# Performance work log

Hardware: AMD Instinct MI355X
Metric: run time of the kernel (lower is better)

## Reference

```python
import jax, jax.numpy as jnp
import numpy as np

H, W = 480, 640
N, Q, K = 128, 8192, 10
MIN_DEPTH = 0.1


def setup_inputs() -> dict:
    key = jax.random.key(0)
    ks = jax.random.split(key, 8)
    pred_depth = jax.random.uniform(ks[0], (1, H, W), jnp.float32, 0.5, 10.0)
    gt_depth = jax.random.uniform(ks[1], (1, H, W), jnp.float32, 0.0, 10.0)
    gt_masks = jax.random.uniform(ks[2], (N, H, W)) > 0.5
    random_mask = jax.random.uniform(ks[3], (N, H, W)) > 0.95  # matches torch.rand>0.95
    k_matrix = jnp.array([[500.0, 0.0, W / 2.0], [0.0, 500.0, H / 2.0], [0.0, 0.0, 1.0]], jnp.float32)
    xq = jax.random.randint(ks[4], (N, Q), 0, H, jnp.int32)
    yq = jax.random.randint(ks[5], (N, Q), 0, W, jnp.int32)
    xp = jax.random.randint(ks[6], (N, K), 0, H, jnp.int32)
    yp = jax.random.randint(ks[7], (N, K), 0, W, jnp.int32)
    return {"pred_depth": pred_depth, "gt_masks": gt_masks, "gt_depth": gt_depth,
            "k_matrix": k_matrix, "random_mask": random_mask,
            "xq": xq, "yq": yq, "xp": xp, "yp": yp}


def reference(pred_depth, gt_masks, gt_depth, k_matrix, random_mask, xq, yq, xp, yp):
    sg = jax.lax.stop_gradient
    d0 = pred_depth[0]  # [H, W]
    fx, fy = k_matrix[0, 0], k_matrix[1, 1]
    u0 = jnp.float32(W // 2)
    v0 = jnp.float32(H // 2)
    u_u0 = jnp.arange(W, dtype=jnp.float32)[None, :] - u0  # [1, W]
    v_v0 = jnp.arange(H, dtype=jnp.float32)[:, None] - v0  # [H, 1]
    # point cloud pw: [H, W, 3]
    px_map = u_u0 * jnp.abs(d0) / fx
    py_map = v_v0 * jnp.abs(d0) / fy
    pw = jnp.stack([px_map, py_map, d0], axis=-1)

    # candidate weights per mask: gt_mask & (rand>0.95) & (gt_depth > min_depth)
    valid = gt_depth[0] > MIN_DEPTH  # [H, W]
    w = (gt_masks & random_mask & valid[None]).astype(jnp.float32)  # [N, H, W]

    # weighted least-squares plane fit z = a*x + b*y + d  (normal equations, same as (A^T A)^-1 A^T b)
    feat = jnp.stack([px_map, py_map, jnp.ones_like(d0)], axis=-1)  # [H, W, 3]
    M = jnp.einsum('nhw,hwi,hwj->nij', w, feat, feat)  # [N, 3, 3]
    rhs = jnp.einsum('nhw,hwi,hw->ni', w, feat, d0)    # [N, 3]
    cnt = w.sum(axis=(1, 2))
    ok = (jnp.abs(jnp.linalg.det(M)) > 1e-8) & (cnt >= 3.0)  # emulate try/except skip
    M_safe = jnp.where(ok[:, None, None], M, jnp.eye(3, dtype=M.dtype))
    fit = sg(jnp.linalg.solve(M_safe, rhs[..., None])[..., 0])  # [N, 3]; detached (numpy in original)
    a, b, d = fit[:, 0:1], fit[:, 1:2], fit[:, 2:3]

    # gather query / propagated point coordinates (detached in original)
    qx = sg(pw[xq, yq, 0])  # [N, Q]
    qy = sg(pw[xq, yq, 1])
    ppx = sg(pw[xp, yp, 0])  # [N, K]
    ppy = sg(pw[xp, yp, 1])
    pd = d0[xp, yp]          # [N, K], grads flow through these depths

    num = a * qx + b * qy + d   # [N, Q]
    den = a * ppx + b * ppy + d  # [N, K]
    vals = num * jnp.mean(pd / den, axis=1, keepdims=True)  # [N, Q]

    # sequential scatter per mask (later masks overwrite earlier, as in the loop)
    def step(out, t):
        xi, yi, vi, oki = t
        cur = out[xi, yi]
        out = out.at[xi, yi].set(jnp.where(oki, vi, cur))
        return out, None

    out, _ = jax.lax.scan(step, d0, (xq, yq, vals, ok))
    return out[None]
```

## Files before the change

### kernel.cpp

```cpp
#include <hip/hip_runtime.h>

#define H_ 480
#define W_ 640
#define HW 307200
#define NN 128
#define QQ 8192
#define KK 10
#define G_ 6
#define PIXB 6144

#define WS_FLAG   0
#define WS_ACC    64
#define WS_ABD    8192
#define WS_VBITS  16384
#define WS_PRIO   65536
#define WS_PACK   1294336
#define WS_NEED   (WS_PACK + (size_t)NN * 4800 * 8)

__global__ __launch_bounds__(256) void prep_k(const unsigned int* __restrict__ gm,
                                              const float* __restrict__ gtd,
                                              unsigned long long* __restrict__ vbits,
                                              int* __restrict__ prio,
                                              float* __restrict__ acc,
                                              int* __restrict__ flag)
{
    const int pix = blockIdx.x * 256 + threadIdx.x;
    prio[pix] = 0;
    if (pix < NN * 12) acc[pix] = 0.0f;
    const bool v = gtd[pix] > 0.1f;
    const unsigned long long b = __ballot(v);
    if ((threadIdx.x & 63) == 0) vbits[pix >> 6] = b;

    if (blockIdx.x == 0) {
        __shared__ int sf;
        if (threadIdx.x == 0) sf = 0;
        __syncthreads();
        int f = 0;
        for (int i = threadIdx.x; i < 4096; i += 256) {
            const unsigned int w = gm[i];
            if (w == 0x3F800000u) f |= 2;
            else if (w > 1u) f |= 1;
        }
        if (f) atomicOr(&sf, f);
        __syncthreads();
        if (threadIdx.x == 0) *flag = (sf & 2) ? 2 : ((sf & 1) ? 1 : 0);
    }
}

__global__ __launch_bounds__(256, 4) void compress_k(
    const void* __restrict__ gmv,
    const void* __restrict__ rmv,
    const int* __restrict__ flag,
    const unsigned long long* __restrict__ vbits,
    unsigned char* __restrict__ packed)
{
    const int n = blockIdx.y;
    const int fmt = *flag;
    const unsigned char* __restrict__ vb8 = (const unsigned char*)vbits;
    unsigned char* __restrict__ outp = packed + (size_t)n * 38400;
    const int g0 = blockIdx.x * 768 + (int)threadIdx.x;

    if (fmt != 1) {
        const unsigned* gp = (const unsigned*)gmv + (size_t)n * HW;
        const unsigned* rp = (const unsigned*)rmv + (size_t)n * HW;
        uint4 ga0[3], ga1[3], ra0[3], ra1[3];
        unsigned char vbb[3];
        #pragma unroll
        for (int k = 0; k < 3; ++k) {
            const int px = (g0 + k * 256) * 8;
            ga0[k] = *reinterpret_cast<const uint4*>(gp + px);
            ga1[k] = *reinterpret_cast<const uint4*>(gp + px + 4);
            ra0[k] = *reinterpret_cast<const uint4*>(rp + px);
            ra1[k] = *reinterpret_cast<const uint4*>(rp + px + 4);
        }
        #pragma unroll
        for (int k = 0; k < 3; ++k) vbb[k] = vb8[g0 + k * 256];
        __builtin_amdgcn_sched_barrier(0);
        #pragma unroll
        for (int k = 0; k < 3; ++k) {
            const unsigned m =
                  ((ga0[k].x & ra0[k].x) != 0u ? 0x01u : 0u)
                | ((ga0[k].y & ra0[k].y) != 0u ? 0x02u : 0u)
                | ((ga0[k].z & ra0[k].z) != 0u ? 0x04u : 0u)
                | ((ga0[k].w & ra0[k].w) != 0u ? 0x08u : 0u)
                | ((ga1[k].x & ra1[k].x) != 0u ? 0x10u : 0u)
                | ((ga1[k].y & ra1[k].y) != 0u ? 0x20u : 0u)
                | ((ga1[k].z & ra1[k].z) != 0u ? 0x40u : 0u)
                | ((ga1[k].w & ra1[k].w) != 0u ? 0x80u : 0u);
            outp[g0 + k * 256] = (unsigned char)(m & vbb[k]);
        }
    } else {
        const unsigned char* gp = (const unsigned char*)gmv + (size_t)n * HW;
        const unsigned char* rp = (const unsigned char*)rmv + (size_t)n * HW;
        unsigned long long ga[3], ra[3];
        unsigned char vbb[3];
        #pragma unroll
        for (int k = 0; k < 3; ++k) {
            const int px = (g0 + k * 256) * 8;
            ga[k] = *reinterpret_cast<const unsigned long long*>(gp + px);
            ra[k] = *reinterpret_cast<const unsigned long long*>(rp + px);
        }
        #pragma unroll
        for (int k = 0; k < 3; ++k) vbb[k] = vb8[g0 + k * 256];
        __builtin_amdgcn_sched_barrier(0);
        #pragma unroll
        for (int k = 0; k < 3; ++k) {
            const unsigned long long ab = ga[k] & ra[k];
            unsigned m = 0;
            #pragma unroll
            for (int j = 0; j < 8; ++j)
                m |= (unsigned)(((ab >> (8*j)) & 0xFFull) != 0) << j;
            outp[g0 + k * 256] = (unsigned char)(m & vbb[k]);
        }
    }
}

__global__ __launch_bounds__(192) void reduce2_k(
    const float* __restrict__ d0,
    const unsigned long long* __restrict__ packed,
    const float* __restrict__ km,
    float* __restrict__ acc)
{
    const int n = blockIdx.y;
    const int w = blockIdx.x * 192 + (int)threadIdx.x;
    unsigned long long bits = packed[(size_t)n * 4800 + w];
    const float rfx = 1.0f / km[0], rfy = 1.0f / km[4];

    float s0=0.f,s1=0.f,s2=0.f,s3=0.f,s4=0.f,s5=0.f,s6=0.f,s7=0.f,s8=0.f;
    if (bits) {
        const int r = w / 10;
        const int c0 = (w - r * 10) * 64;
        const float pyb = (float)(r - 240) * rfy;
        const float* drow = d0 + r * W_ + c0;
        while (bits) {
            const int j = __ffsll((unsigned long long)bits) - 1;
            bits &= bits - 1;
            const float d = drow[j];
            const float ad = fabsf(d);
            const float px = (float)(c0 + j - 320) * ad * rfx;
            const float py = pyb * ad;
            s0 += px*px; s1 += px*py; s2 += px;
            s3 += py*py; s4 += py;    s5 += 1.0f;
            s6 += px*d;  s7 += py*d;  s8 += d;
        }
    }

    float s[9] = {s0,s1,s2,s3,s4,s5,s6,s7,s8};
    #pragma unroll
    for (int off = 32; off > 0; off >>= 1) {
        #pragma unroll
        for (int i = 0; i < 9; ++i) s[i] += __shfl_down(s[i], off);
    }
    __shared__ float ls[3][9];
    const int wave = threadIdx.x >> 6, lane = threadIdx.x & 63;
    if (lane == 0) {
        #pragma unroll
        for (int i = 0; i < 9; ++i) ls[wave][i] = s[i];
    }
    __syncthreads();
    if (threadIdx.x < 9) {
        const int i = threadIdx.x;
        atomicAdd(&acc[n*12 + i], ls[0][i] + ls[1][i] + ls[2][i]);
    }
}

__global__ __launch_bounds__(256) void reduce_k(
    const float* __restrict__ d0,
    const void* __restrict__ gmv,
    const void* __restrict__ rmv,
    const float* __restrict__ km,
    const int* __restrict__ flag,
    const unsigned long long* __restrict__ vbits,
    float* __restrict__ acc)
{
    const int n = blockIdx.y;
    const int base = blockIdx.x * PIXB + (int)threadIdx.x * 4;
    const int fmt = *flag;
    const float rfx = 1.0f / km[0], rfy = 1.0f / km[4];
    const size_t moff = (size_t)n * HW;

    unsigned bitsArr[G_];
    if (fmt != 1) {
        uint4 ga[G_], ra[G_];
        #pragma unroll
        for (int g = 0; g < G_; ++g) {
            const int p = base + g * 1024;
            ga[g] = *reinterpret_cast<const uint4*>((const unsigned*)gmv + moff + p);
            ra[g] = *reinterpret_cast<const uint4*>((const unsigned*)rmv + moff + p);
        }
        #pragma unroll
        for (int g = 0; g < G_; ++g) {
            bitsArr[g] = ((ga[g].x & ra[g].x) != 0u ? 1u : 0u)
                       | ((ga[g].y & ra[g].y) != 0u ? 2u : 0u)
                       | ((ga[g].z & ra[g].z) != 0u ? 4u : 0u)
                       | ((ga[g].w & ra[g].w) != 0u ? 8u : 0u);
        }
    } else {
        unsigned ga[G_], ra[G_];
        #pragma unroll
        for (int g = 0; g < G_; ++g) {
            const int p = base + g * 1024;
            ga[g] = *reinterpret_cast<const unsigned*>((const unsigned char*)gmv + moff + p);
            ra[g] = *reinterpret_cast<const unsigned*>((const unsigned char*)rmv + moff + p);
        }
        #pragma unroll
        for (int g = 0; g < G_; ++g) {
            const unsigned ab = ga[g] & ra[g];
            bitsArr[g] = (unsigned)((ab & 0xFFu) != 0) | ((unsigned)(((ab>>8) & 0xFFu) != 0) << 1)
                       | ((unsigned)(((ab>>16) & 0xFFu) != 0) << 2) | ((unsigned)((ab>>24) != 0) << 3);
        }
    }

    float s0=0.f,s1=0.f,s2=0.f,s3=0.f,s4=0.f,s5=0.f,s6=0.f,s7=0.f,s8=0.f;
    #pragma unroll
    for (int g = 0; g < G_; ++g) {
        const int p0 = base + g * 1024;
        unsigned bits = bitsArr[g] & ((unsigned)(vbits[p0 >> 6] >> (p0 & 63)) & 0xFu);
        if (bits) {
            const float4 dv = *reinterpret_cast<const float4*>(d0 + p0);
            const int r = p0 / W_;
            const int c0 = p0 - r * W_;
            const float pyb = (float)(r - 240) * rfy;
            while (bits) {
                const int j = __ffs(bits) - 1;
                bits &= bits - 1;
                const float d = (j == 0) ? dv.x : (j == 1) ? dv.y : (j == 2) ? dv.z : dv.w;
                const float ad = fabsf(d);
                const float px = (float)(c0 + j - 320) * ad * rfx;
                const float py = pyb * ad;
                s0 += px*px; s1 += px*py; s2 += px;
                s3 += py*py; s4 += py;    s5 += 1.0f;
                s6 += px*d;  s7 += py*d;  s8 += d;
            }
        }
    }

    float s[9] = {s0,s1,s2,s3,s4,s5,s6,s7,s8};
    #pragma unroll
    for (int off = 32; off > 0; off >>= 1) {
        #pragma unroll
        for (int i = 0; i < 9; ++i) s[i] += __shfl_down(s[i], off);
    }
    __shared__ float ls[4][9];
    const int wave = threadIdx.x >> 6, lane = threadIdx.x & 63;
    if (lane == 0) {
        #pragma unroll
        for (int i = 0; i < 9; ++i) ls[wave][i] = s[i];
    }
    __syncthreads();
    if (threadIdx.x == 0) {
        #pragma unroll
        for (int i = 0; i < 9; ++i)
            atomicAdd(&acc[n*12 + i], ls[0][i] + ls[1][i] + ls[2][i] + ls[3][i]);
    }
}

__global__ void solve_k(const float* __restrict__ acc,
                        const float* __restrict__ d0,
                        const float* __restrict__ km,
                        const int* __restrict__ xp,
                        const int* __restrict__ yp,
                        float* __restrict__ abd)
{
    const int n = blockIdx.x * blockDim.x + threadIdx.x;
    if (n >= NN) return;
    const float* s = acc + n * 12;
    const double M00=s[0], M01=s[1], M02=s[2], M11=s[3], M12=s[4], M22=s[5];
    const double r0=s[6], r1=s[7], r2=s[8];
    const double cnt = M22;
    const double c00 = M11*M22 - M12*M12;
    const double c01 = M01*M22 - M12*M02;
    const double c02 = M01*M12 - M11*M02;
    const double det = M00*c00 - M01*c01 + M02*c02;
    const bool ok = (fabs(det) > 1e-8) && (cnt >= 3.0);
    float a = 0.f, b = 0.f, dc = 0.f, scale = 0.f;
    if (ok) {
        const double inv = 1.0 / det;
        const double t1 = r1*M22 - r2*M12;
        const double t2 = M01*r2 - r1*M02;
        const double x0 = (r0*c00 - M01*t1 + M02*(r1*M12 - r2*M11)) * inv;
        const double x1 = (M00*t1 - r0*c01 + M02*t2) * inv;
        const double x2 = (M00*(M11*r2 - r1*M12) - M01*t2 + r0*c02) * inv;
        a = (float)x0; b = (float)x1; dc = (float)x2;
        const float fx = km[0], fy = km[4];
        float sum = 0.0f;
        for (int k = 0; k < KK; ++k) {
            const int xi = xp[n*KK + k], yi = yp[n*KK + k];
            const float dd = d0[xi * W_ + yi];
            const float ad = fabsf(dd);
            const float ppx = (float)(yi - 320) * ad / fx;
            const float ppy = (float)(xi - 240) * ad / fy;
            const float den = a * ppx + b * ppy + dc;
            sum += dd / den;
        }
        scale = sum / (float)KK;
    }
    abd[n*8+0] = a; abd[n*8+1] = b; abd[n*8+2] = dc;
    abd[n*8+3] = scale;
    abd[n*8+4] = ok ? 1.0f : 0.0f;
}

__global__ __launch_bounds__(256) void prio_k(const int* __restrict__ xq,
                                              const int* __restrict__ yq,
                                              const float* __restrict__ abd,
                                              int* __restrict__ prio)
{
    const int idx = (blockIdx.x * 256 + threadIdx.x) * 4;
    const int n = idx >> 13;
    if (abd[n*8+4] == 0.0f) return;
    const int4 xs = *reinterpret_cast<const int4*>(xq + idx);
    const int4 ys = *reinterpret_cast<const int4*>(yq + idx);
    const int np = n + 1;
    atomicMax(prio + xs.x * W_ + ys.x, np);
    atomicMax(prio + xs.y * W_ + ys.y, np);
    atomicMax(prio + xs.z * W_ + ys.z, np);
    atomicMax(prio + xs.w * W_ + ys.w, np);
}

__global__ __launch_bounds__(256) void final_k(const int* __restrict__ prio,
                                               const float* __restrict__ abd,
                                               const float* __restrict__ d0,
                                               const float* __restrict__ km,
                                               float* __restrict__ out)
{
    const int p0 = (blockIdx.x * 256 + threadIdx.x) * 4;
    const int4 pr4 = *reinterpret_cast<const int4*>(prio + p0);
    const float4 dv = *reinterpret_cast<const float4*>(d0 + p0);
    const float rfx = 1.0f / km[0], rfy = 1.0f / km[4];
    const int r = p0 / W_;
    const int c0 = p0 - r * W_;
    const float yv = (float)(r - 240) * rfy;
    const int pr[4] = {pr4.x, pr4.y, pr4.z, pr4.w};
    const float dd[4] = {dv.x, dv.y, dv.z, dv.w};
    float o[4];
    #pragma unroll
    for (int j = 0; j < 4; ++j) {
        float v = dd[j];
        if (pr[j] > 0) {
            const int n = pr[j] - 1;
            const float ad = fabsf(dd[j]);
            const float qx = (float)(c0 + j - 320) * ad * rfx;
            const float qy = yv * ad;
            v = (abd[n*8+0]*qx + abd[n*8+1]*qy + abd[n*8+2]) * abd[n*8+3];
        }
        o[j] = v;
    }
    *reinterpret_cast<float4*>(out + p0) = make_float4(o[0], o[1], o[2], o[3]);
}

extern "C" void kernel_launch(void* const* d_in, const int* in_sizes, int n_in,
                              void* d_out, int out_size, void* d_ws, size_t ws_size,
                              hipStream_t stream)
{
    const float* d0  = (const float*)d_in[0];
    const void*  gm  = d_in[1];
    const float* gtd = (const float*)d_in[2];
    const float* km  = (const float*)d_in[3];
    const void*  rm  = d_in[4];
    const int*   xq  = (const int*)d_in[5];
    const int*   yq  = (const int*)d_in[6];
    const int*   xp  = (const int*)d_in[7];
    const int*   yp  = (const int*)d_in[8];
    float* out = (float*)d_out;
    char*  ws  = (char*)d_ws;

    int* flag = (int*)(ws + WS_FLAG);
    float* acc = (float*)(ws + WS_ACC);
    float* abd = (float*)(ws + WS_ABD);
    unsigned long long* vbits = (unsigned long long*)(ws + WS_VBITS);
    int* prio = (int*)(ws + WS_PRIO);
    unsigned char* packed = (unsigned char*)(ws + WS_PACK);

    prep_k<<<HW / 256, 256, 0, stream>>>((const unsigned int*)gm, gtd, vbits, prio, acc, flag);
    if (ws_size >= WS_NEED) {
        compress_k<<<dim3(50, NN), 256, 0, stream>>>(gm, rm, flag, vbits, packed);
        reduce2_k<<<dim3(25, NN), 192, 0, stream>>>(d0, (const unsigned long long*)packed, km, acc);
    } else {
        reduce_k<<<dim3(HW / PIXB, NN), 256, 0, stream>>>(d0, gm, rm, km, flag, vbits, acc);
    }
    solve_k<<<2, 64, 0, stream>>>(acc, d0, km, xp, yp, abd);
    prio_k<<<(NN * QQ / 4) / 256, 256, 0, stream>>>(xq, yq, abd, prio);
    final_k<<<(HW / 4) / 256, 256, 0, stream>>>(prio, abd, d0, km, out);
}
```

Measured before the change: 124.5 us.

## Restructure mask compression to nibble bytes with inline-asm staged loads

compress_k now has each thread handle 4 contiguous pixels per group, storing one nibble byte per group instead of a full 8-pixel byte. Its mask loads are issued as explicit global_load_dwordx4 instructions with staged s_waitcnt so computation overlaps outstanding loads, and the valid-bit AND is moved from compress into reduce2_k. reduce2_k reads 16 bytes of nibbles and packs them into a 64-bit mask before applying vbits. The packed buffer doubles in size and the grid grows to 75 blocks per mask. The aim is more fully coalesced loads and better latency hiding in the bandwidth-bound pass, at the cost of more intermediate traffic and extra bit manipulation in reduce2_k.

Result: no change. 126.2 us (+1.4%).

```diff
diff --git a/kernel.cpp b/kernel.cpp
--- a/kernel.cpp
+++ b/kernel.cpp
@@ -15,7 +15,7 @@
 #define WS_VBITS  16384
 #define WS_PRIO   65536
 #define WS_PACK   1294336
-#define WS_NEED   (WS_PACK + (size_t)NN * 4800 * 8)
+#define WS_NEED   (WS_PACK + (size_t)NN * 76800)
 
 __global__ __launch_bounds__(256) void prep_k(const unsigned int* __restrict__ gm,
                                               const float* __restrict__ gtd,
@@ -47,84 +47,97 @@
     }
 }
 
+__device__ __forceinline__ unsigned nib4(const uint4& a, const uint4& b)
+{
+    return ((a.x & b.x) ? 1u : 0u) | ((a.y & b.y) ? 2u : 0u)
+         | ((a.z & b.z) ? 4u : 0u) | ((a.w & b.w) ? 8u : 0u);
+}
+
 __global__ __launch_bounds__(256, 4) void compress_k(
     const void* __restrict__ gmv,
     const void* __restrict__ rmv,
     const int* __restrict__ flag,
-    const unsigned long long* __restrict__ vbits,
     unsigned char* __restrict__ packed)
 {
     const int n = blockIdx.y;
+    const int tid = (int)threadIdx.x;
     const int fmt = *flag;
-    const unsigned char* __restrict__ vb8 = (const unsigned char*)vbits;
-    unsigned char* __restrict__ outp = packed + (size_t)n * 38400;
-    const int g0 = blockIdx.x * 768 + (int)threadIdx.x;
+    unsigned char* __restrict__ outp = packed + (size_t)n * 76800 + blockIdx.x * 1024 + tid;
 
     if (fmt != 1) {
-        const unsigned* gp = (const unsigned*)gmv + (size_t)n * HW;
-        const unsigned* rp = (const unsigned*)rmv + (size_t)n * HW;
-        uint4 ga0[3], ga1[3], ra0[3], ra1[3];
-        unsigned char vbb[3];
-        #pragma unroll
-        for (int k = 0; k < 3; ++k) {
-            const int px = (g0 + k * 256) * 8;
-            ga0[k] = *reinterpret_cast<const uint4*>(gp + px);
-            ga1[k] = *reinterpret_cast<const uint4*>(gp + px + 4);
-            ra0[k] = *reinterpret_cast<const uint4*>(rp + px);
-            ra1[k] = *reinterpret_cast<const uint4*>(rp + px + 4);
-        }
-        #pragma unroll
-        for (int k = 0; k < 3; ++k) vbb[k] = vb8[g0 + k * 256];
+        const unsigned* gp = (const unsigned*)gmv + (size_t)n * HW + blockIdx.x * 4096 + tid * 4;
+        const unsigned* rp = (const unsigned*)rmv + (size_t)n * HW + blockIdx.x * 4096 + tid * 4;
+        uint4 a0, a1, a2, a3, b0, b1, b2, b3;
+        asm volatile(
+            "global_load_dwordx4 %[va0], %[pg0], off\n\t"
+            "global_load_dwordx4 %[vb0], %[pr0], off\n\t"
+            "global_load_dwordx4 %[va1], %[pg1], off\n\t"
+            "global_load_dwordx4 %[vb1], %[pr1], off\n\t"
+            "global_load_dwordx4 %[va2], %[pg2], off\n\t"
+            "global_load_dwordx4 %[vb2], %[pr2], off\n\t"
+            "global_load_dwordx4 %[va3], %[pg3], off\n\t"
+            "global_load_dwordx4 %[vb3], %[pr3], off"
+            : [va0]"=&v"(a0), [vb0]"=&v"(b0), [va1]"=&v"(a1), [vb1]"=&v"(b1),
+              [va2]"=&v"(a2), [vb2]"=&v"(b2), [va3]"=&v"(a3), [vb3]"=&v"(b3)
+            : [pg0]"v"(gp),        [pr0]"v"(rp),
+              [pg1]"v"(gp + 1024), [pr1]"v"(rp + 1024),
+              [pg2]"v"(gp + 2048), [pr2]"v"(rp + 2048),
+              [pg3]"v"(gp + 3072), [pr3]"v"(rp + 3072)
+            : "memory");
+        asm volatile("s_waitcnt vmcnt(6)" ::: "memory");
         __builtin_amdgcn_sched_barrier(0);
-        #pragma unroll
-        for (int k = 0; k < 3; ++k) {
-            const unsigned m =
-                  ((ga0[k].x & ra0[k].x) != 0u ? 0x01u : 0u)
-                | ((ga0[k].y & ra0[k].y) != 0u ? 0x02u : 0u)
-                | ((ga0[k].z & ra0[k].z) != 0u ? 0x04u : 0u)
-                | ((ga0[k].w & ra0[k].w) != 0u ? 0x08u : 0u)
-                | ((ga1[k].x & ra1[k].x) != 0u ? 0x10u : 0u)
-                | ((ga1[k].y & ra1[k].y) != 0u ? 0x20u : 0u)
-                | ((ga1[k].z & ra1[k].z) != 0u ? 0x40u : 0u)
-                | ((ga1[k].w & ra1[k].w) != 0u ? 0x80u : 0u);
-            outp[g0 + k * 256] = (unsigned char)(m & vbb[k]);
-        }
+        const unsigned m0 = nib4(a0, b0);
+        asm volatile("s_waitcnt vmcnt(4)" ::: "memory");
+        __builtin_amdgcn_sched_barrier(0);
+        const unsigned m1 = nib4(a1, b1);
+        asm volatile("s_waitcnt vmcnt(2)" ::: "memory");
+        __builtin_amdgcn_sched_barrier(0);
+        const unsigned m2 = nib4(a2, b2);
+        asm volatile("s_waitcnt vmcnt(0)" ::: "memory");
+        __builtin_amdgcn_sched_barrier(0);
+        const unsigned m3 = nib4(a3, b3);
+        outp[0]   = (unsigned char)m0;
+        outp[256] = (unsigned char)m1;
+        outp[512] = (unsigned char)m2;
+        outp[768] = (unsigned char)m3;
     } else {
         const unsigned char* gp = (const unsigned char*)gmv + (size_t)n * HW;
         const unsigned char* rp = (const unsigned char*)rmv + (size_t)n * HW;
-        unsigned long long ga[3], ra[3];
-        unsigned char vbb[3];
-        #pragma unroll
-        for (int k = 0; k < 3; ++k) {
-            const int px = (g0 + k * 256) * 8;
-            ga[k] = *reinterpret_cast<const unsigned long long*>(gp + px);
-            ra[k] = *reinterpret_cast<const unsigned long long*>(rp + px);
-        }
-        #pragma unroll
-        for (int k = 0; k < 3; ++k) vbb[k] = vb8[g0 + k * 256];
-        __builtin_amdgcn_sched_barrier(0);
-        #pragma unroll
-        for (int k = 0; k < 3; ++k) {
-            const unsigned long long ab = ga[k] & ra[k];
-            unsigned m = 0;
-            #pragma unroll
-            for (int j = 0; j < 8; ++j)
-                m |= (unsigned)(((ab >> (8*j)) & 0xFFull) != 0) << j;
-            outp[g0 + k * 256] = (unsigned char)(m & vbb[k]);
+        #pragma unroll
+        for (int g = 0; g < 4; ++g) {
+            const int px = blockIdx.x * 4096 + g * 1024 + tid * 4;
+            const unsigned a = *reinterpret_cast<const unsigned*>(gp + px);
+            const unsigned b = *reinterpret_cast<const unsigned*>(rp + px);
+            const unsigned ab = a & b;
+            const unsigned m = (unsigned)((ab & 0xFFu) != 0)
+                             | ((unsigned)(((ab >> 8) & 0xFFu) != 0) << 1)
+                             | ((unsigned)(((ab >> 16) & 0xFFu) != 0) << 2)
+                             | ((unsigned)((ab >> 24) != 0) << 3);
+            outp[g * 256] = (unsigned char)m;
         }
     }
 }
 
 __global__ __launch_bounds__(192) void reduce2_k(
     const float* __restrict__ d0,
-    const unsigned long long* __restrict__ packed,
+    const unsigned char* __restrict__ packed,
+    const unsigned long long* __restrict__ vbits,
     const float* __restrict__ km,
     float* __restrict__ acc)
 {
     const int n = blockIdx.y;
     const int w = blockIdx.x * 192 + (int)threadIdx.x;
-    unsigned long long bits = packed[(size_t)n * 4800 + w];
+    const uint4 pk = *reinterpret_cast<const uint4*>(packed + (size_t)n * 76800 + w * 16);
     const float rfx = 1.0f / km[0], rfy = 1.0f / km[4];
+
+    unsigned t0 = pk.x; t0 = (t0 | (t0 >> 4)) & 0x00FF00FFu; t0 = (t0 | (t0 >> 8)) & 0xFFFFu;
+    unsigned t1 = pk.y; t1 = (t1 | (t1 >> 4)) & 0x00FF00FFu; t1 = (t1 | (t1 >> 8)) & 0xFFFFu;
+    unsigned t2 = pk.z; t2 = (t2 | (t2 >> 4)) & 0x00FF00FFu; t2 = (t2 | (t2 >> 8)) & 0xFFFFu;
+    unsigned t3 = pk.w; t3 = (t3 | (t3 >> 4)) & 0x00FF00FFu; t3 = (t3 | (t3 >> 8)) & 0xFFFFu;
+    unsigned long long bits =
+        (unsigned long long)t0 | ((unsigned long long)t1 << 16)
+      | ((unsigned long long)t2 << 32) | ((unsigned long long)t3 << 48);
+    bits &= vbits[w];
 
     float s0=0.f,s1=0.f,s2=0.f,s3=0.f,s4=0.f,s5=0.f,s6=0.f,s7=0.f,s8=0.f;
     if (bits) {
@@ -189,12 +202,7 @@
             ra[g] = *reinterpret_cast<const uint4*>((const unsigned*)rmv + moff + p);
         }
         #pragma unroll
-        for (int g = 0; g < G_; ++g) {
-            bitsArr[g] = ((ga[g].x & ra[g].x) != 0u ? 1u : 0u)
-                       | ((ga[g].y & ra[g].y) != 0u ? 2u : 0u)
-                       | ((ga[g].z & ra[g].z) != 0u ? 4u : 0u)
-                       | ((ga[g].w & ra[g].w) != 0u ? 8u : 0u);
-        }
+        for (int g = 0; g < G_; ++g) bitsArr[g] = nib4(ga[g], ra[g]);
     } else {
         unsigned ga[G_], ra[G_];
         #pragma unroll
@@ -373,8 +381,8 @@
 
     prep_k<<<HW / 256, 256, 0, stream>>>((const unsigned int*)gm, gtd, vbits, prio, acc, flag);
     if (ws_size >= WS_NEED) {
-        compress_k<<<dim3(50, NN), 256, 0, stream>>>(gm, rm, flag, vbits, packed);
-        reduce2_k<<<dim3(25, NN), 192, 0, stream>>>(d0, (const unsigned long long*)packed, km, acc);
+        compress_k<<<dim3(75, NN), 256, 0, stream>>>(gm, rm, flag, packed);
+        reduce2_k<<<dim3(25, NN), 192, 0, stream>>>(d0, packed, vbits, km, acc);
     } else {
         reduce_k<<<dim3(HW / PIXB, NN), 256, 0, stream>>>(d0, gm, rm, km, flag, vbits, acc);
     }
```

## Rewrite mask compression as grid-stride loop with nontemporal 16B loads

Applied to the files above, without the earlier changes.

The mask-compression kernel moves from a 2D per-mask grid, where each thread issued many wide loads, to a flat 2048-block grid-stride loop. Each thread loads one 16-byte vector of each mask with nontemporal hints, and adjacent lanes combine their nibbles through a shuffle. The goal is a more streaming, coalesced read of the large float-format masks that avoids polluting the cache. In exchange, each thread has less memory-level parallelism, half the lanes sit idle on the byte stores, and an extra modulo is computed for the valid-bits lookup.

Measured after the change: 119.9 us. -3.7%, faster.

```diff
diff --git a/kernel.cpp b/kernel.cpp
--- a/kernel.cpp
+++ b/kernel.cpp
@@ -15,7 +15,9 @@
 #define WS_VBITS  16384
 #define WS_PRIO   65536
 #define WS_PACK   1294336
-#define WS_NEED   (WS_PACK + (size_t)NN * 4800 * 8)
+#define WS_NEED   (WS_PACK + (size_t)NN * 38400)
+
+typedef unsigned int u32x4 __attribute__((ext_vector_type(4)));
 
 __global__ __launch_bounds__(256) void prep_k(const unsigned int* __restrict__ gm,
                                               const float* __restrict__ gtd,
@@ -47,70 +49,55 @@
     }
 }
 
-__global__ __launch_bounds__(256, 4) void compress_k(
+__device__ __forceinline__ unsigned nib4v(const u32x4 a, const u32x4 b)
+{
+    return ((a.x & b.x) ? 1u : 0u) | ((a.y & b.y) ? 2u : 0u)
+         | ((a.z & b.z) ? 4u : 0u) | ((a.w & b.w) ? 8u : 0u);
+}
+
+__device__ __forceinline__ unsigned nib4(const uint4& a, const uint4& b)
+{
+    return ((a.x & b.x) ? 1u : 0u) | ((a.y & b.y) ? 2u : 0u)
+         | ((a.z & b.z) ? 4u : 0u) | ((a.w & b.w) ? 8u : 0u);
+}
+
+__global__ __launch_bounds__(256) void compress_k(
     const void* __restrict__ gmv,
     const void* __restrict__ rmv,
     const int* __restrict__ flag,
     const unsigned long long* __restrict__ vbits,
     unsigned char* __restrict__ packed)
 {
-    const int n = blockIdx.y;
     const int fmt = *flag;
     const unsigned char* __restrict__ vb8 = (const unsigned char*)vbits;
-    unsigned char* __restrict__ outp = packed + (size_t)n * 38400;
-    const int g0 = blockIdx.x * 768 + (int)threadIdx.x;
+    const int tid0 = blockIdx.x * 256 + (int)threadIdx.x;
+    const int stride = 2048 * 256;
+    const unsigned lane = threadIdx.x & 63u;
 
     if (fmt != 1) {
-        const unsigned* gp = (const unsigned*)gmv + (size_t)n * HW;
-        const unsigned* rp = (const unsigned*)rmv + (size_t)n * HW;
-        uint4 ga0[3], ga1[3], ra0[3], ra1[3];
-        unsigned char vbb[3];
-        #pragma unroll
-        for (int k = 0; k < 3; ++k) {
-            const int px = (g0 + k * 256) * 8;
-            ga0[k] = *reinterpret_cast<const uint4*>(gp + px);
-            ga1[k] = *reinterpret_cast<const uint4*>(gp + px + 4);
-            ra0[k] = *reinterpret_cast<const uint4*>(rp + px);
-            ra1[k] = *reinterpret_cast<const uint4*>(rp + px + 4);
-        }
-        #pragma unroll
-        for (int k = 0; k < 3; ++k) vbb[k] = vb8[g0 + k * 256];
-        __builtin_amdgcn_sched_barrier(0);
-        #pragma unroll
-        for (int k = 0; k < 3; ++k) {
-            const unsigned m =
-                  ((ga0[k].x & ra0[k].x) != 0u ? 0x01u : 0u)
-                | ((ga0[k].y & ra0[k].y) != 0u ? 0x02u : 0u)
-                | ((ga0[k].z & ra0[k].z) != 0u ? 0x04u : 0u)
-                | ((ga0[k].w & ra0[k].w) != 0u ? 0x08u : 0u)
-                | ((ga1[k].x & ra1[k].x) != 0u ? 0x10u : 0u)
-                | ((ga1[k].y & ra1[k].y) != 0u ? 0x20u : 0u)
-                | ((ga1[k].z & ra1[k].z) != 0u ? 0x40u : 0u)
-                | ((ga1[k].w & ra1[k].w) != 0u ? 0x80u : 0u);
-            outp[g0 + k * 256] = (unsigned char)(m & vbb[k]);
+        const u32x4* __restrict__ gp = (const u32x4*)gmv;
+        const u32x4* __restrict__ rp = (const u32x4*)rmv;
+        for (int i = tid0; i < NN * HW / 4; i += stride) {
+            const u32x4 a = __builtin_nontemporal_load(gp + i);
+            const u32x4 b = __builtin_nontemporal_load(rp + i);
+            const unsigned m = nib4v(a, b);
+            const unsigned hi = __shfl_down(m, 1);
+            if (!(lane & 1u)) {
+                const int g = i >> 1;
+                packed[g] = (unsigned char)((m | (hi << 4)) & vb8[g % 38400]);
+            }
         }
     } else {
-        const unsigned char* gp = (const unsigned char*)gmv + (size_t)n * HW;
-        const unsigned char* rp = (const unsigned char*)rmv + (size_t)n * HW;
-        unsigned long long ga[3], ra[3];
-        unsigned char vbb[3];
-        #pragma unroll
-        for (int k = 0; k < 3; ++k) {
-            const int px = (g0 + k * 256) * 8;
-            ga[k] = *reinterpret_cast<const unsigned long long*>(gp + px);
-            ra[k] = *reinterpret_cast<const unsigned long long*>(rp + px);
-        }
-        #pragma unroll
-        for (int k = 0; k < 3; ++k) vbb[k] = vb8[g0 + k * 256];
-        __builtin_amdgcn_sched_barrier(0);
-        #pragma unroll
-        for (int k = 0; k < 3; ++k) {
-            const unsigned long long ab = ga[k] & ra[k];
+        const unsigned long long* __restrict__ gp = (const unsigned long long*)gmv;
+        const unsigned long long* __restrict__ rp = (const unsigned long long*)rmv;
+        for (int g = tid0; g < NN * HW / 8; g += stride) {
+            const unsigned long long ab = __builtin_nontemporal_load(gp + g)
+                                        & __builtin_nontemporal_load(rp + g);
             unsigned m = 0;
             #pragma unroll
             for (int j = 0; j < 8; ++j)
                 m |= (unsigned)(((ab >> (8*j)) & 0xFFull) != 0) << j;
-            outp[g0 + k * 256] = (unsigned char)(m & vbb[k]);
+            packed[g] = (unsigned char)(m & vb8[g % 38400]);
         }
     }
 }
@@ -189,12 +176,7 @@
             ra[g] = *reinterpret_cast<const uint4*>((const unsigned*)rmv + moff + p);
         }
         #pragma unroll
-        for (int g = 0; g < G_; ++g) {
-            bitsArr[g] = ((ga[g].x & ra[g].x) != 0u ? 1u : 0u)
-                       | ((ga[g].y & ra[g].y) != 0u ? 2u : 0u)
-                       | ((ga[g].z & ra[g].z) != 0u ? 4u : 0u)
-                       | ((ga[g].w & ra[g].w) != 0u ? 8u : 0u);
-        }
+        for (int g = 0; g < G_; ++g) bitsArr[g] = nib4(ga[g], ra[g]);
     } else {
         unsigned ga[G_], ra[G_];
         #pragma unroll
@@ -373,7 +355,7 @@
 
     prep_k<<<HW / 256, 256, 0, stream>>>((const unsigned int*)gm, gtd, vbits, prio, acc, flag);
     if (ws_size >= WS_NEED) {
-        compress_k<<<dim3(50, NN), 256, 0, stream>>>(gm, rm, flag, vbits, packed);
+        compress_k<<<2048, 256, 0, stream>>>(gm, rm, flag, vbits, packed);
         reduce2_k<<<dim3(25, NN), 192, 0, stream>>>(d0, (const unsigned long long*)packed, km, acc);
     } else {
         reduce_k<<<dim3(HW / PIXB, NN), 256, 0, stream>>>(d0, gm, rm, km, flag, vbits, acc);
```
